# Kernel tuning notes

Measured on AMD Instinct MI355X. Metric: run time of the kernel, lower is better.

## Reference

```python
import jax, jax.numpy as jnp
import numpy as np
from jax import lax

B, H, W, CIN, COUT, LAT = 8, 128, 128, 256, 256, 512


def lrelu(x):
    return jax.nn.leaky_relu(x, 0.2)


def setup_inputs() -> dict:
    key = jax.random.key(0)
    ks = jax.random.split(key, 9)
    inp = {
        "data": jax.random.normal(ks[0], (B, H, W, CIN), jnp.float32),
        "latent": jax.random.normal(ks[1], (B, LAT), jnp.float32),
        "noise": jax.random.normal(ks[2], (B, H, W, COUT), jnp.float32),
        # ScaledDense std_dense: LAT -> CIN, bias init ones
        "std_W": jax.random.normal(ks[3], (LAT, CIN), jnp.float32),
        "std_b": jnp.ones((CIN,), jnp.float32),
        # 3x3 conv weights (HWIO), N(0,1) init; scaled at call time
        "conv_w": jax.random.normal(ks[4], (3, 3, CIN, COUT), jnp.float32),
        "bias": jnp.zeros((1, 1, 1, COUT), jnp.float32),
        "noise_coef": jnp.zeros((1, 1, 1, COUT), jnp.float32),
        # pointwise denses: COUT -> 4*COUT -> COUT
        "D1_W": jax.random.normal(ks[5], (COUT, 4 * COUT), jnp.float32),
        "D1_b": jnp.zeros((4 * COUT,), jnp.float32),
        "D2_W": jax.random.normal(ks[6], (4 * COUT, COUT), jnp.float32),
        "D2_b": jnp.zeros((COUT,), jnp.float32),
    }
    return inp


def reference(data, latent, noise, std_W, std_b, conv_w, bias, noise_coef,
              D1_W, D1_b, D2_W, D2_b):
    lat_dim = latent.shape[-1]
    cin = conv_w.shape[2]
    cout = conv_w.shape[3]
    # equalized-LR scaled dense: style vector s [B, Cin]
    s = latent @ (std_W * np.float32(np.sqrt(2.0 / lat_dim))) + std_b
    # modulate input channels
    x = data * s[:, None, None, :]
    # scaled 3x3 conv, SAME padding
    w = conv_w * np.float32(np.sqrt(2.0 / (cin * 9)))
    y = lax.conv_general_dilated(
        x, w, window_strides=(1, 1), padding="SAME",
        dimension_numbers=("NHWC", "HWIO", "NHWC"))
    # demodulation: d[b,o] = rsqrt(sum_{k,i} (w[k,i,o]*s[b,i])^2 + eps)
    # computed as small matmul on squared quantities (no [B,3,3,Cin,Cout] tensor)
    w2 = jnp.sum(w * w, axis=(0, 1))                      # [Cin, Cout]
    d = lax.rsqrt(jnp.einsum("io,bi->bo", w2, s * s) + 1e-8)  # [B, Cout]
    y = y * d[:, None, None, :] + bias + noise * noise_coef
    y = lrelu(y)
    h = lrelu(y @ (D1_W * np.float32(np.sqrt(2.0 / cout))) + D1_b)
    out = lrelu(h @ (D2_W * np.float32(np.sqrt(2.0 / (4 * cout)))) + D2_b)
    return out
```

## Files before the change

kernel.cpp:

```cpp
#include <hip/hip_runtime.h>

typedef unsigned short ushort_t;
typedef __attribute__((ext_vector_type(8))) short short8;
typedef __attribute__((ext_vector_type(4))) float f32x4;

#define C1 0.0625f
#define C2 0.029462782549439483f
#define C2SQ (2.0f/2304.0f)
#define C3 0.08838834764831845f
#define C4 0.04419417382415922f

__device__ __forceinline__ float bf2f(ushort_t u) {
  union { unsigned int i; float f; } v; v.i = ((unsigned int)u) << 16; return v.f;
}
__device__ __forceinline__ ushort_t f2bf(float f) {
  union { float f; unsigned int i; } v; v.f = f;
  unsigned int r = v.i + 0x7fffu + ((v.i >> 16) & 1u);
  return (ushort_t)(r >> 16);
}
__device__ __forceinline__ void async16(const void* g, void* l) {
  __builtin_amdgcn_global_load_lds(
      (const __attribute__((address_space(1))) unsigned int*)g,
      (__attribute__((address_space(3))) unsigned int*)l, 16, 0, 0);
}
__device__ __forceinline__ float lrelu(float v) { return v > 0.f ? v : 0.2f * v; }

__global__ void k_style(const float* __restrict__ latent, const float* __restrict__ stdW,
                        const float* __restrict__ stdb, float* __restrict__ s) {
  __shared__ float red[256];
  int b = blockIdx.x, ic = blockIdx.y;
  int il = threadIdx.x & 31, lp = threadIdx.x >> 5;
  int i = (ic << 5) + il;
  float acc = 0.f;
  int l0 = lp << 6;
  for (int l = l0; l < l0 + 64; ++l)
    acc += latent[(b << 9) + l] * stdW[(l << 8) + i];
  red[threadIdx.x] = acc;
  __syncthreads();
  if (lp == 0) {
    float v = 0.f;
#pragma unroll
    for (int p = 0; p < 8; ++p) v += red[(p << 5) + il];
    s[(b << 8) + i] = v * C1 + stdb[i];
  }
}

__global__ void k_w2(const float* __restrict__ convw, float* __restrict__ w2) {
  int t = blockIdx.x * 256 + threadIdx.x;
  float acc = 0.f;
#pragma unroll
  for (int tap = 0; tap < 9; ++tap) {
    float w = convw[tap * 65536 + t];
    acc += w * w;
  }
  w2[t] = acc * C2SQ;
}

__global__ void k_demod(const float* __restrict__ w2, const float* __restrict__ s,
                        float* __restrict__ dm) {
  __shared__ float red[256];
  int b = blockIdx.x, oc = blockIdx.y;
  int ol = threadIdx.x & 31, ip = threadIdx.x >> 5;
  int o = (oc << 5) + ol;
  float acc = 0.f;
  int i0 = ip << 5;
  for (int i = i0; i < i0 + 32; ++i) {
    float si = s[(b << 8) + i];
    acc += w2[(i << 8) + o] * si * si;
  }
  red[threadIdx.x] = acc;
  __syncthreads();
  if (ip == 0) {
    float v = 1e-8f;
#pragma unroll
    for (int p = 0; p < 8; ++p) v += red[(p << 5) + ol];
    dm[(b << 8) + o] = rsqrtf(v);
  }
}

__global__ void k_wt(const float* __restrict__ convw, ushort_t* __restrict__ wt) {
  int t = blockIdx.x * 256 + threadIdx.x;
  int o = t / 2304;
  int kk = t - o * 2304;
  int tap = kk >> 8, i = kk & 255;
  wt[t] = f2bf(convw[tap * 65536 + (i << 8) + o] * C2);
}

__global__ void k_w1t(const float* __restrict__ d1w, ushort_t* __restrict__ w1t) {
  int t = blockIdx.x * 256 + threadIdx.x;
  int n = t >> 8, k = t & 255;
  w1t[t] = f2bf(d1w[(k << 10) + n] * C3);
}
__global__ void k_w2t(const float* __restrict__ d2w, ushort_t* __restrict__ w2t) {
  int t = blockIdx.x * 256 + threadIdx.x;
  int o = t >> 10, k = t & 1023;
  w2t[t] = f2bf(d2w[(k << 8) + o] * C4);
}

__global__ void k_pad(const float* __restrict__ data, const float* __restrict__ s,
                      ushort_t* __restrict__ xs) {
  int tid = blockIdx.x * 256 + threadIdx.x;
  int ci8 = tid & 31;
  int p = tid >> 5;
  int xp = p % 130;
  int q = p / 130;
  int yp = q % 130;
  int b = q / 130;
  short8 ov = {0, 0, 0, 0, 0, 0, 0, 0};
  if (yp >= 1 && yp <= 128 && xp >= 1 && xp <= 128) {
    const f32x4* src = (const f32x4*)(data + ((((b << 7) + (yp - 1)) << 7) + (xp - 1)) * 256 + (ci8 << 3));
    const f32x4* sp  = (const f32x4*)(s + (b << 8) + (ci8 << 3));
    f32x4 v0 = src[0], v1 = src[1];
    f32x4 s0 = sp[0],  s1 = sp[1];
#pragma unroll
    for (int j = 0; j < 4; ++j) ov[j]     = (short)f2bf(v0[j] * s0[j]);
#pragma unroll
    for (int j = 0; j < 4; ++j) ov[4 + j] = (short)f2bf(v1[j] * s1[j]);
  }
  *(short8*)(xs + ((size_t)tid << 3)) = ov;
}

__global__ __launch_bounds__(256) void k_conv(
    const ushort_t* __restrict__ xs, const ushort_t* __restrict__ wt,
    const float* __restrict__ dmod, const float* __restrict__ bias,
    const float* __restrict__ ncoef, const float* __restrict__ noise,
    ushort_t* __restrict__ y) {
  __shared__ __align__(16) ushort_t a_lds[2][128 * 32];
  __shared__ __align__(16) ushort_t b_lds[2][128 * 32];
  int rb = blockIdx.x;
  int n0 = blockIdx.y << 7;
  int b = rb >> 7, yr = rb & 127;
  int t = threadIdx.x;
  int lane = t & 63;
  int wm = (t >> 7) & 1, wn = (t >> 6) & 1;
  const ushort_t* ximg = xs + (size_t)b * (130 * 130 * 256);

  const f32x4 fz = {0.f, 0.f, 0.f, 0.f};
  f32x4 acc[4][4];
#pragma unroll
  for (int i = 0; i < 4; ++i) {
#pragma unroll
    for (int j = 0; j < 4; ++j) acc[i][j] = fz;
  }

#pragma unroll 1
  for (int tap = 0; tap < 9; ++tap) {
    int ky = tap / 3;
    int kx = tap - ky * 3;
    const ushort_t* arow = ximg + ((yr + ky) * 130 + kx) * 256;
#pragma unroll 1
    for (int cp = 0; cp < 4; ++cp) {
#pragma unroll
      for (int h = 0; h < 2; ++h) {
        int k0 = ((cp << 1) + h) << 5;
#pragma unroll
        for (int r = 0; r < 2; ++r) {
          int flat = t + (r << 8);
          int m = flat >> 2, k8 = (flat & 3) << 3;
          async16(arow + m * 256 + k0 + k8, &a_lds[h][flat << 3]);
        }
#pragma unroll
        for (int r = 0; r < 2; ++r) {
          int flat = t + (r << 8);
          int n = flat >> 2, k8 = (flat & 3) << 3;
          async16(wt + (size_t)(n0 + n) * 2304 + tap * 256 + k0 + k8, &b_lds[h][flat << 3]);
        }
      }
      __syncthreads();
#pragma unroll
      for (int h = 0; h < 2; ++h) {
        short8 af[4], bfr[4];
#pragma unroll
        for (int i = 0; i < 4; ++i) {
          af[i]  = *(const short8*)&a_lds[h][((wm << 6) + (i << 4) + (lane & 15)) * 32 + ((lane >> 4) << 3)];
          bfr[i] = *(const short8*)&b_lds[h][((wn << 6) + (i << 4) + (lane & 15)) * 32 + ((lane >> 4) << 3)];
        }
#pragma unroll
        for (int i = 0; i < 4; ++i) {
#pragma unroll
          for (int j = 0; j < 4; ++j)
            acc[i][j] = __builtin_amdgcn_mfma_f32_16x16x32_bf16(af[i], bfr[j], acc[i][j], 0, 0, 0);
        }
      }
      __syncthreads();
    }
  }

  int prow = rb << 7;
#pragma unroll
  for (int j = 0; j < 4; ++j) {
    int o = n0 + (wn << 6) + (j << 4) + (lane & 15);
    float dv = dmod[(b << 8) + o];
    float bv = bias[o];
    float nc = ncoef[o];
#pragma unroll
    for (int i = 0; i < 4; ++i) {
      int mbase = (wm << 6) + (i << 4) + ((lane >> 4) << 2);
#pragma unroll
      for (int r = 0; r < 4; ++r) {
        int idx = (prow + mbase + r) * 256 + o;
        float v = acc[i][j][r] * dv + bv + noise[idx] * nc;
        y[idx] = f2bf(lrelu(v));
      }
    }
  }
}

__global__ __launch_bounds__(256, 2) void k_dense(
    const ushort_t* __restrict__ y, float* __restrict__ out,
    const ushort_t* __restrict__ w1t, const float* __restrict__ b1,
    const ushort_t* __restrict__ w2t, const float* __restrict__ b2) {
  __shared__ __align__(16) ushort_t a1[2][128 * 32];
  __shared__ __align__(16) ushort_t bb[256 * 32];
  __shared__ __align__(16) ushort_t ly[128 * 136];
  int rb = blockIdx.x;
  int t = threadIdx.x, lane = t & 63;
  int wm = (t >> 7) & 1, wn = (t >> 6) & 1;
  int row0 = rb << 7;

  const f32x4 fz = {0.f, 0.f, 0.f, 0.f};
  f32x4 oacc[4][8];
#pragma unroll
  for (int i = 0; i < 4; ++i) {
#pragma unroll
    for (int j = 0; j < 8; ++j) oacc[i][j] = fz;
  }

#pragma unroll 1
  for (int nc = 0; nc < 8; ++nc) {
    f32x4 hacc[4][4];
#pragma unroll
    for (int i = 0; i < 4; ++i) {
#pragma unroll
      for (int j = 0; j < 4; ++j) hacc[i][j] = fz;
    }
#pragma unroll 1
    for (int kp = 0; kp < 4; ++kp) {
#pragma unroll
      for (int h = 0; h < 2; ++h) {
        int k0 = ((kp << 1) + h) << 5;
#pragma unroll
        for (int r = 0; r < 2; ++r) {
          int flat = t + (r << 8);
          int m = flat >> 2, k8 = (flat & 3) << 3;
          async16(y + (row0 + m) * 256 + k0 + k8, &a1[h][flat << 3]);
          async16(w1t + ((nc << 7) + m) * 256 + k0 + k8, &bb[(h << 12) + (flat << 3)]);
        }
      }
      __syncthreads();
#pragma unroll
      for (int h = 0; h < 2; ++h) {
        short8 af[4], bfr[4];
#pragma unroll
        for (int i = 0; i < 4; ++i) {
          af[i]  = *(const short8*)&a1[h][((wm << 6) + (i << 4) + (lane & 15)) * 32 + ((lane >> 4) << 3)];
          bfr[i] = *(const short8*)&bb[(h << 12) + ((wn << 6) + (i << 4) + (lane & 15)) * 32 + ((lane >> 4) << 3)];
        }
#pragma unroll
        for (int i = 0; i < 4; ++i) {
#pragma unroll
          for (int j = 0; j < 4; ++j)
            hacc[i][j] = __builtin_amdgcn_mfma_f32_16x16x32_bf16(af[i], bfr[j], hacc[i][j], 0, 0, 0);
        }
      }
      __syncthreads();
    }
#pragma unroll
    for (int j = 0; j < 4; ++j) {
      int n = (wn << 6) + (j << 4) + (lane & 15);
      float bv = b1[(nc << 7) + n];
#pragma unroll
      for (int i = 0; i < 4; ++i) {
        int mbase = (wm << 6) + (i << 4) + ((lane >> 4) << 2);
#pragma unroll
        for (int r = 0; r < 4; ++r)
          ly[(mbase + r) * 136 + n] = f2bf(lrelu(hacc[i][j][r] + bv));
      }
    }
    __syncthreads();
#pragma unroll 1
    for (int kc2 = 0; kc2 < 4; ++kc2) {
      int kk0 = kc2 << 5;
#pragma unroll
      for (int r = 0; r < 4; ++r) {
        int flat = t + (r << 8);
        int o = flat >> 2, k8 = (flat & 3) << 3;
        async16(w2t + o * 1024 + (nc << 7) + kk0 + k8, &bb[flat << 3]);
      }
      __syncthreads();
      short8 af2[4];
#pragma unroll
      for (int i = 0; i < 4; ++i)
        af2[i] = *(const short8*)&ly[((wm << 6) + (i << 4) + (lane & 15)) * 136 + kk0 + ((lane >> 4) << 3)];
#pragma unroll
      for (int j = 0; j < 8; ++j) {
        short8 bfr2 = *(const short8*)&bb[((wn << 7) + (j << 4) + (lane & 15)) * 32 + ((lane >> 4) << 3)];
#pragma unroll
        for (int i = 0; i < 4; ++i)
          oacc[i][j] = __builtin_amdgcn_mfma_f32_16x16x32_bf16(af2[i], bfr2, oacc[i][j], 0, 0, 0);
      }
      __syncthreads();
    }
  }
#pragma unroll
  for (int j = 0; j < 8; ++j) {
    int o = (wn << 7) + (j << 4) + (lane & 15);
    float bv = b2[o];
#pragma unroll
    for (int i = 0; i < 4; ++i) {
      int mbase = (wm << 6) + (i << 4) + ((lane >> 4) << 2);
#pragma unroll
      for (int r = 0; r < 4; ++r)
        out[(row0 + mbase + r) * 256 + o] = lrelu(oacc[i][j][r] + bv);
    }
  }
}

extern "C" void kernel_launch(void* const* d_in, const int* in_sizes, int n_in,
                              void* d_out, int out_size, void* d_ws, size_t ws_size,
                              hipStream_t stream) {
  const float* data   = (const float*)d_in[0];
  const float* latent = (const float*)d_in[1];
  const float* noise  = (const float*)d_in[2];
  const float* stdW   = (const float*)d_in[3];
  const float* stdb   = (const float*)d_in[4];
  const float* convw  = (const float*)d_in[5];
  const float* bias   = (const float*)d_in[6];
  const float* ncoef  = (const float*)d_in[7];
  const float* D1W    = (const float*)d_in[8];
  const float* D1b    = (const float*)d_in[9];
  const float* D2W    = (const float*)d_in[10];
  const float* D2b    = (const float*)d_in[11];
  float* out = (float*)d_out;

  char* ws = (char*)d_ws;
  float*    s    = (float*)ws;
  float*    dmod = (float*)(ws + 8192);
  float*    w2   = (float*)(ws + 16384);
  ushort_t* wt   = (ushort_t*)(ws + 278528);
  ushort_t* w1t  = (ushort_t*)(ws + 1458176);
  ushort_t* w2t  = (ushort_t*)(ws + 1982464);
  ushort_t* xs   = (ushort_t*)(ws + 2506752);
  ushort_t* yv   = (ushort_t*)(ws + 71729152);

  k_style<<<dim3(8, 8), 256, 0, stream>>>(latent, stdW, stdb, s);
  k_w2<<<256, 256, 0, stream>>>(convw, w2);
  k_demod<<<dim3(8, 8), 256, 0, stream>>>(w2, s, dmod);
  k_wt<<<2304, 256, 0, stream>>>(convw, wt);
  k_w1t<<<1024, 256, 0, stream>>>(D1W, w1t);
  k_w2t<<<1024, 256, 0, stream>>>(D2W, w2t);
  k_pad<<<16900, 256, 0, stream>>>(data, s, xs);
  k_conv<<<dim3(1024, 2), 256, 0, stream>>>(xs, wt, dmod, bias, ncoef, noise, yv);
  k_dense<<<1024, 256, 0, stream>>>(yv, out, w1t, D1b, w2t, D2b);
}
```

Measured before the change: 795.6 us.

## Rewrite conv as 256x256-tile pipelined GEMM with swizzled LDS and double buffering

The implicit-GEMM conv kernel now uses 512-thread blocks, each computing a 256-row by 256-channel output tile (two image rows, all output channels) with K steps of 64. It double-buffers XOR-swizzled LDS tiles and interleaves async global-to-LDS loads for the next K step with MFMA work on the current one, using explicit vmcnt waits, barriers and setprio. Block IDs are remapped across groups of eight. The aim is to remove the per-step load-then-sync stalls, cut LDS bank conflicts, and reuse each A and B tile across more MFMAs. In exchange it needs much more LDS (128 KB) and many accumulator registers, and its hand-counted waitcnt and barrier schedule is fragile.

Result: faster. 703.5 us (-11.6%).

```diff
diff --git a/kernel.cpp b/kernel.cpp
--- a/kernel.cpp
+++ b/kernel.cpp
@@ -120,90 +120,171 @@
   *(short8*)(xs + ((size_t)tid << 3)) = ov;
 }
 
-__global__ __launch_bounds__(256) void k_conv(
+
+#define SWZ_FLAT(flat, row) ((((flat) ^ (row)) & 7) << 3)
+
+__device__ __forceinline__ void stage_a(const ushort_t* ximg, int y0, int h, int kt2,
+                                        int t, ushort_t* dst) {
+  int tap = kt2 >> 2;
+  int ci0 = (kt2 & 3) << 6;
+  int ky = (tap >= 6) ? 2 : (tap >= 3 ? 1 : 0);
+  int kx = tap - ky * 3;
+  const ushort_t* ga = ximg + ((y0 + h + ky) * 130 + kx) * 256 + ci0;
+#pragma unroll
+  for (int is = 0; is < 2; ++is) {
+    int flat = t + (is << 9);
+    int row = flat >> 3;
+    int cil = SWZ_FLAT(flat, row);
+    async16(ga + row * 256 + cil, dst + (flat << 3));
+  }
+}
+
+__device__ __forceinline__ void stage_b(const ushort_t* wtp, int h, int kt2, int t, ushort_t* dst) {
+  const ushort_t* gb = wtp + (kt2 << 6) + (size_t)(h << 7) * 2304;
+#pragma unroll
+  for (int is = 0; is < 2; ++is) {
+    int flat = t + (is << 9);
+    int row = flat >> 3;
+    int cil = SWZ_FLAT(flat, row);
+    async16(gb + (size_t)row * 2304 + cil, dst + (flat << 3));
+  }
+}
+
+#define LOAD_A(BASE) {                                                        \
+  _Pragma("unroll") for (int q = 0; q < 4; ++q) {                             \
+    int lr = (wm << 6) + (q << 4) + (lane & 15);                              \
+    int bo0 = (lr << 7) + ((lane >> 4) << 4);                                 \
+    int sw = (lr & 7) << 4;                                                   \
+    af[q][0] = *(const short8*)((BASE) + ((bo0      ) ^ sw));                 \
+    af[q][1] = *(const short8*)((BASE) + ((bo0 + 64 ) ^ sw)); } }
+
+#define LOAD_B(BASE, BF) {                                                    \
+  _Pragma("unroll") for (int p = 0; p < 2; ++p) {                             \
+    int lr = (wn << 5) + (p << 4) + (lane & 15);                              \
+    int bo0 = (lr << 7) + ((lane >> 4) << 4);                                 \
+    int sw = (lr & 7) << 4;                                                   \
+    BF[p][0] = *(const short8*)((BASE) + ((bo0      ) ^ sw));                 \
+    BF[p][1] = *(const short8*)((BASE) + ((bo0 + 64 ) ^ sw)); } }
+
+#define MFMA_BLK(MH, NH, BF) {                                                \
+  _Pragma("unroll") for (int q = 0; q < 4; ++q)                               \
+    _Pragma("unroll") for (int p = 0; p < 2; ++p)                             \
+      _Pragma("unroll") for (int ks = 0; ks < 2; ++ks)                        \
+        acc[MH][NH][q][p] = __builtin_amdgcn_mfma_f32_16x16x32_bf16(          \
+            af[q][ks], BF[p][ks], acc[MH][NH][q][p], 0, 0, 0); }
+
+#define PH_BAR()  __builtin_amdgcn_s_barrier()
+#define PH_LGKM() asm volatile("s_waitcnt lgkmcnt(0)" ::: "memory")
+#define VM4()     asm volatile("s_waitcnt vmcnt(4)" ::: "memory")
+#define PRIO1()   __builtin_amdgcn_s_setprio(1)
+#define PRIO0()   __builtin_amdgcn_s_setprio(0)
+
+__global__ __launch_bounds__(512, 2) void k_conv(
     const ushort_t* __restrict__ xs, const ushort_t* __restrict__ wt,
     const float* __restrict__ dmod, const float* __restrict__ bias,
     const float* __restrict__ ncoef, const float* __restrict__ noise,
     ushort_t* __restrict__ y) {
-  __shared__ __align__(16) ushort_t a_lds[2][128 * 32];
-  __shared__ __align__(16) ushort_t b_lds[2][128 * 32];
-  int rb = blockIdx.x;
-  int n0 = blockIdx.y << 7;
-  int b = rb >> 7, yr = rb & 127;
+  __shared__ __align__(16) ushort_t lds[2][4][128 * 64];
+
+  int bid0 = blockIdx.x;
+  int bid = (bid0 & 7) * 64 + (bid0 >> 3);
+  int m0 = bid << 8;
+  int b = m0 >> 14;
+  int y0 = (m0 & 16383) >> 7;
+  const ushort_t* ximg = xs + (size_t)b * (130 * 130 * 256);
+
   int t = threadIdx.x;
   int lane = t & 63;
-  int wm = (t >> 7) & 1, wn = (t >> 6) & 1;
-  const ushort_t* ximg = xs + (size_t)b * (130 * 130 * 256);
+  int wid = t >> 6;
+  int wm = wid >> 2, wn = wid & 3;
 
   const f32x4 fz = {0.f, 0.f, 0.f, 0.f};
-  f32x4 acc[4][4];
-#pragma unroll
-  for (int i = 0; i < 4; ++i) {
-#pragma unroll
-    for (int j = 0; j < 4; ++j) acc[i][j] = fz;
-  }
+  f32x4 acc[2][2][4][2];
+#pragma unroll
+  for (int a0 = 0; a0 < 2; ++a0)
+#pragma unroll
+    for (int a1 = 0; a1 < 2; ++a1)
+#pragma unroll
+      for (int a2 = 0; a2 < 4; ++a2)
+#pragma unroll
+        for (int a3 = 0; a3 < 2; ++a3) acc[a0][a1][a2][a3] = fz;
+
+  short8 af[4][2], bf[2][2], bg[2][2];
+
+  stage_a(ximg, y0, 0, 0, t, &lds[0][0][0]);
+  stage_b(wt,        0, 0, t, &lds[0][2][0]);
+  stage_b(wt,        1, 0, t, &lds[0][3][0]);
+  stage_a(ximg, y0, 1, 0, t, &lds[0][1][0]);
 
 #pragma unroll 1
-  for (int tap = 0; tap < 9; ++tap) {
-    int ky = tap / 3;
-    int kx = tap - ky * 3;
-    const ushort_t* arow = ximg + ((yr + ky) * 130 + kx) * 256;
-#pragma unroll 1
-    for (int cp = 0; cp < 4; ++cp) {
-#pragma unroll
-      for (int h = 0; h < 2; ++h) {
-        int k0 = ((cp << 1) + h) << 5;
-#pragma unroll
-        for (int r = 0; r < 2; ++r) {
-          int flat = t + (r << 8);
-          int m = flat >> 2, k8 = (flat & 3) << 3;
-          async16(arow + m * 256 + k0 + k8, &a_lds[h][flat << 3]);
+  for (int kt = 0; kt < 35; ++kt) {
+    int cb = kt & 1, nb = cb ^ 1;
+    const char* a0b = (const char*)&lds[cb][0][0];
+    const char* a1b = (const char*)&lds[cb][1][0];
+    const char* b0b = (const char*)&lds[cb][2][0];
+    const char* b1b = (const char*)&lds[cb][3][0];
+    int kt2 = kt + 1;
+    VM4(); PH_BAR();
+    LOAD_A(a0b); LOAD_B(b0b, bf);
+    stage_a(ximg, y0, 0, kt2, t, &lds[nb][0][0]);
+    PH_BAR(); PH_LGKM();
+    PRIO1(); MFMA_BLK(0, 0, bf); PRIO0();
+    VM4(); PH_BAR();
+    LOAD_B(b1b, bg);
+    stage_b(wt, 0, kt2, t, &lds[nb][2][0]);
+    PH_BAR(); PH_LGKM();
+    PRIO1(); MFMA_BLK(0, 1, bg); PRIO0();
+    VM4(); PH_BAR();
+    LOAD_A(a1b);
+    stage_b(wt, 1, kt2, t, &lds[nb][3][0]);
+    PH_BAR(); PH_LGKM();
+    PRIO1(); MFMA_BLK(1, 1, bg); PRIO0();
+    stage_a(ximg, y0, 1, kt2, t, &lds[nb][1][0]);
+    PH_BAR();
+    PRIO1(); MFMA_BLK(1, 0, bf); PRIO0();
+  }
+  {
+    const char* a0b = (const char*)&lds[1][0][0];
+    const char* a1b = (const char*)&lds[1][1][0];
+    const char* b0b = (const char*)&lds[1][2][0];
+    const char* b1b = (const char*)&lds[1][3][0];
+    asm volatile("s_waitcnt vmcnt(4)" ::: "memory"); PH_BAR();
+    LOAD_A(a0b); LOAD_B(b0b, bf);
+    PH_BAR(); PH_LGKM();
+    PRIO1(); MFMA_BLK(0, 0, bf); PRIO0();
+    asm volatile("s_waitcnt vmcnt(2)" ::: "memory"); PH_BAR();
+    LOAD_B(b1b, bg);
+    PH_BAR(); PH_LGKM();
+    PRIO1(); MFMA_BLK(0, 1, bg); PRIO0();
+    asm volatile("s_waitcnt vmcnt(0)" ::: "memory"); PH_BAR();
+    LOAD_A(a1b);
+    PH_BAR(); PH_LGKM();
+    PRIO1(); MFMA_BLK(1, 1, bg); PRIO0();
+    PH_BAR();
+    PRIO1(); MFMA_BLK(1, 0, bf); PRIO0();
+  }
+
+#pragma unroll
+  for (int mh = 0; mh < 2; ++mh)
+#pragma unroll
+    for (int nh = 0; nh < 2; ++nh)
+#pragma unroll
+      for (int p = 0; p < 2; ++p) {
+        int o = (nh << 7) + (wn << 5) + (p << 4) + (lane & 15);
+        float dv = dmod[(b << 8) + o];
+        float bv = bias[o];
+        float nc = ncoef[o];
+#pragma unroll
+        for (int q = 0; q < 4; ++q) {
+          int mloc = (mh << 7) + (wm << 6) + (q << 4) + ((lane >> 4) << 2);
+#pragma unroll
+          for (int r = 0; r < 4; ++r) {
+            int idx = (m0 + mloc + r) * 256 + o;
+            float v = acc[mh][nh][q][p][r] * dv + bv + noise[idx] * nc;
+            y[idx] = f2bf(lrelu(v));
+          }
         }
-#pragma unroll
-        for (int r = 0; r < 2; ++r) {
-          int flat = t + (r << 8);
-          int n = flat >> 2, k8 = (flat & 3) << 3;
-          async16(wt + (size_t)(n0 + n) * 2304 + tap * 256 + k0 + k8, &b_lds[h][flat << 3]);
-        }
-      }
-      __syncthreads();
-#pragma unroll
-      for (int h = 0; h < 2; ++h) {
-        short8 af[4], bfr[4];
-#pragma unroll
-        for (int i = 0; i < 4; ++i) {
-          af[i]  = *(const short8*)&a_lds[h][((wm << 6) + (i << 4) + (lane & 15)) * 32 + ((lane >> 4) << 3)];
-          bfr[i] = *(const short8*)&b_lds[h][((wn << 6) + (i << 4) + (lane & 15)) * 32 + ((lane >> 4) << 3)];
-        }
-#pragma unroll
-        for (int i = 0; i < 4; ++i) {
-#pragma unroll
-          for (int j = 0; j < 4; ++j)
-            acc[i][j] = __builtin_amdgcn_mfma_f32_16x16x32_bf16(af[i], bfr[j], acc[i][j], 0, 0, 0);
-        }
-      }
-      __syncthreads();
-    }
-  }
-
-  int prow = rb << 7;
-#pragma unroll
-  for (int j = 0; j < 4; ++j) {
-    int o = n0 + (wn << 6) + (j << 4) + (lane & 15);
-    float dv = dmod[(b << 8) + o];
-    float bv = bias[o];
-    float nc = ncoef[o];
-#pragma unroll
-    for (int i = 0; i < 4; ++i) {
-      int mbase = (wm << 6) + (i << 4) + ((lane >> 4) << 2);
-#pragma unroll
-      for (int r = 0; r < 4; ++r) {
-        int idx = (prow + mbase + r) * 256 + o;
-        float v = acc[i][j][r] * dv + bv + noise[idx] * nc;
-        y[idx] = f2bf(lrelu(v));
-      }
-    }
-  }
+      }
 }
 
 __global__ __launch_bounds__(256, 2) void k_dense(
@@ -350,6 +431,6 @@
   k_w1t<<<1024, 256, 0, stream>>>(D1W, w1t);
   k_w2t<<<1024, 256, 0, stream>>>(D2W, w2t);
   k_pad<<<16900, 256, 0, stream>>>(data, s, xs);
-  k_conv<<<dim3(1024, 2), 256, 0, stream>>>(xs, wt, dmod, bias, ncoef, noise, yv);
+  k_conv<<<512, 512, 0, stream>>>(xs, wt, dmod, bias, ncoef, noise, yv);
   k_dense<<<1024, 256, 0, stream>>>(yv, out, w1t, D1b, w2t, D2b);
 }
```
